# Kernel optimization log

Measured on AMD Instinct MI355X. Metric: run time of the kernel, lower is better.

Reference implementation:

```python
import jax, jax.numpy as jnp
import numpy as np

EMBED = 64
HEADS = 8
HEAD_DIM = EMBED // HEADS
B, N, T = 8, 128, 64


def setup_inputs() -> dict:
    key = jax.random.key(0)
    ks = jax.random.split(key, 8)
    shp = (B, N, T, EMBED)
    values = jax.random.normal(ks[0], shp, dtype=jnp.float32)
    keys = jax.random.normal(ks[1], shp, dtype=jnp.float32)
    query = jax.random.normal(ks[2], shp, dtype=jnp.float32)
    s = 1.0 / np.sqrt(HEAD_DIM)
    Wv = jax.random.normal(ks[3], (HEAD_DIM, HEAD_DIM), dtype=jnp.float32) * s
    Wk = jax.random.normal(ks[4], (HEAD_DIM, HEAD_DIM), dtype=jnp.float32) * s
    Wq = jax.random.normal(ks[5], (HEAD_DIM, HEAD_DIM), dtype=jnp.float32) * s
    so = 1.0 / np.sqrt(EMBED)
    Wo = jax.random.normal(ks[6], (EMBED, EMBED), dtype=jnp.float32) * so
    bo = jax.random.normal(ks[7], (EMBED,), dtype=jnp.float32) * 0.01
    return {"values": values, "keys": keys, "query": query,
            "Wv": Wv, "Wk": Wk, "Wq": Wq, "Wo": Wo, "bo": bo}


def reference(values, keys, query, Wv, Wk, Wq, Wo, bo):
    b, n, t, c = query.shape
    h, d = HEADS, HEAD_DIM
    # split heads: (B,N,T,H,D)
    v = values.reshape(b, n, t, h, d)
    k = keys.reshape(b, n, t, h, d)
    q = query.reshape(b, n, t, h, d)
    # per-head linear projections (torch Linear: x @ W.T, no bias)
    v = jnp.einsum('bnthd,ed->bnthe', v, Wv)
    k = jnp.einsum('bnthd,ed->bnthe', k, Wk)
    q = jnp.einsum('bnthd,ed->bnthe', q, Wq)
    # attention over spatial axis N, independent per (t, h)
    energy = jnp.einsum('bqthd,bkthd->bqkth', q, k)  # (B,N,N,T,H)
    attn = jax.nn.softmax(energy / jnp.sqrt(jnp.float32(c)), axis=2)
    out = jnp.einsum('bqkth,bkthd->bqthd', attn, v).reshape(b, n, t, h * d)
    # fc_out: x @ Wo.T + bo
    return out @ Wo.T + bo
```

## Files before the change

kernel.cpp:

```cpp
#include <hip/hip_runtime.h>


typedef _Float16 half4 __attribute__((ext_vector_type(4)));
typedef float    f32x4 __attribute__((ext_vector_type(4)));

#define MFMA16(a,b,c) __builtin_amdgcn_mfma_f32_16x16x16f16((a),(b),(c),0,0,0)

__device__ __forceinline__ unsigned short f2h(float f){
    union { _Float16 h; unsigned short u; } c; c.h = (_Float16)f; return c.u;
}

#define ZS 0
#define KB 8
#define QB 8200
#define VB 16392
#define CB 24584
#define WB 33288
#define LDS_TOTAL 37640

__global__ __launch_bounds__(512, 4)
void sattn_kernel(const float* __restrict__ V,
                  const float* __restrict__ K,
                  const float* __restrict__ Q,
                  const float* __restrict__ Wv,
                  const float* __restrict__ Wk,
                  const float* __restrict__ Wq,
                  const float* __restrict__ Wo,
                  const float* __restrict__ bo,
                  float* __restrict__ Out)
{
    __shared__ __align__(16) unsigned short smem[LDS_TOTAL];

    const int tid  = threadIdx.x;
    const int bid  = blockIdx.x;
    const int b    = bid >> 6;
    const int t    = bid & 63;
    const long base = (long)b * 524288 + t * 64;
    const float SC = 0.18033688011112043f;

    if (tid < 4) *(unsigned int*)(smem + tid*2) = 0u;

    {
        int o = tid >> 3, c8 = tid & 7;
        const float* ws = Wo + o*64 + c8*8;
        float4 a = *(const float4*)ws;
        float4 d = *(const float4*)(ws + 4);
        half4 h0; h0.x=(_Float16)a.x; h0.y=(_Float16)a.y; h0.z=(_Float16)a.z; h0.w=(_Float16)a.w;
        half4 h1; h1.x=(_Float16)d.x; h1.y=(_Float16)d.y; h1.z=(_Float16)d.z; h1.w=(_Float16)d.w;
        *(half4*)(smem + WB + o*68 + c8*8)     = h0;
        *(half4*)(smem + WB + o*68 + c8*8 + 4) = h1;
    }

    for (int i = 0; i < 2; ++i){
        int id = i*512 + tid;
        int cn = id >> 3, ch = id & 7;
        const float* pk = K + base + cn*4096 + ch*8;
        const float* pv = V + base + cn*4096 + ch*8;
        const float* pq = Q + base + cn*4096 + ch*8;
        float4 ka = *(const float4*)pk, kb = *(const float4*)(pk+4);
        float4 va = *(const float4*)pv, vb = *(const float4*)(pv+4);
        float4 qa = *(const float4*)pq, qb = *(const float4*)(pq+4);
        float ok[8], ov[8], oq[8];
        #pragma unroll
        for (int e = 0; e < 8; ++e){
            float4 wk0 = *(const float4*)(Wk + e*8), wk1 = *(const float4*)(Wk + e*8 + 4);
            float4 wv0 = *(const float4*)(Wv + e*8), wv1 = *(const float4*)(Wv + e*8 + 4);
            float4 wq0 = *(const float4*)(Wq + e*8), wq1 = *(const float4*)(Wq + e*8 + 4);
            ok[e] = ka.x*wk0.x + ka.y*wk0.y + ka.z*wk0.z + ka.w*wk0.w
                  + kb.x*wk1.x + kb.y*wk1.y + kb.z*wk1.z + kb.w*wk1.w;
            ov[e] = va.x*wv0.x + va.y*wv0.y + va.z*wv0.z + va.w*wv0.w
                  + vb.x*wv1.x + vb.y*wv1.y + vb.z*wv1.z + vb.w*wv1.w;
            oq[e] = (qa.x*wq0.x + qa.y*wq0.y + qa.z*wq0.z + qa.w*wq0.w
                  +  qb.x*wq1.x + qb.y*wq1.y + qb.z*wq1.z + qb.w*wq1.w) * SC;
        }
        half4 k0; k0.x=(_Float16)ok[0]; k0.y=(_Float16)ok[1]; k0.z=(_Float16)ok[2]; k0.w=(_Float16)ok[3];
        half4 k1; k1.x=(_Float16)ok[4]; k1.y=(_Float16)ok[5]; k1.z=(_Float16)ok[6]; k1.w=(_Float16)ok[7];
        half4 q0; q0.x=(_Float16)oq[0]; q0.y=(_Float16)oq[1]; q0.z=(_Float16)oq[2]; q0.w=(_Float16)oq[3];
        half4 q1; q1.x=(_Float16)oq[4]; q1.y=(_Float16)oq[5]; q1.z=(_Float16)oq[6]; q1.w=(_Float16)oq[7];
        *(half4*)(smem + KB + ch*1024 + cn*8)     = k0;
        *(half4*)(smem + KB + ch*1024 + cn*8 + 4) = k1;
        *(half4*)(smem + QB + ch*1024 + cn*8)     = q0;
        *(half4*)(smem + QB + ch*1024 + cn*8 + 4) = q1;
        #pragma unroll
        for (int e = 0; e < 8; ++e)
            smem[VB + ch*1024 + e*128 + cn] = f2h(ov[e]);
    }

    __syncthreads();

    const int h    = tid >> 6;
    const int q16  = tid & 15;
    const int quad = (tid & 63) >> 4;
    const f32x4 zz = {0.f, 0.f, 0.f, 0.f};

    half4 kf[8];
    #pragma unroll
    for (int mt = 0; mt < 8; ++mt){
        int a = KB + h*1024 + (mt*16 + q16)*8 + quad*4;
        if (quad >= 2) a = ZS;
        kf[mt] = *(const half4*)(smem + a);
    }
    half4 vf[8];
    #pragma unroll
    for (int s = 0; s < 8; ++s){
        int a = VB + h*1024 + q16*128 + s*16 + quad*4;
        if (q16 >= 8) a = ZS;
        vf[s] = *(const half4*)(smem + a);
    }

    #pragma unroll 1
    for (int qs = 0; qs < 8; ++qs){
        int qa = QB + h*1024 + (qs*16 + q16)*8 + quad*4;
        if (quad >= 2) qa = ZS;
        half4 qf = *(const half4*)(smem + qa);

        f32x4 acc[8];
        #pragma unroll
        for (int mt = 0; mt < 8; ++mt)
            acc[mt] = MFMA16(kf[mt], qf, zz);

        float s = 0.f;
        #pragma unroll
        for (int mt = 0; mt < 8; ++mt){
            #pragma unroll
            for (int r = 0; r < 4; ++r){
                float p = __builtin_amdgcn_exp2f(acc[mt][r]);
                acc[mt][r] = p;
                s += p;
            }
        }
        s += __shfl_xor(s, 16, 64);
        s += __shfl_xor(s, 32, 64);
        float inv = 1.0f / s;

        half4 pf[8];
        #pragma unroll
        for (int mt = 0; mt < 8; ++mt){
            pf[mt].x = (_Float16)(acc[mt][0]*inv);
            pf[mt].y = (_Float16)(acc[mt][1]*inv);
            pf[mt].z = (_Float16)(acc[mt][2]*inv);
            pf[mt].w = (_Float16)(acc[mt][3]*inv);
        }

        f32x4 o = zz;
        #pragma unroll
        for (int s8 = 0; s8 < 8; ++s8)
            o = MFMA16(pf[s8], vf[s8], o);

        if (q16 < 8){
            #pragma unroll
            for (int r = 0; r < 4; ++r){
                int row = qs*16 + quad*4 + r;
                smem[CB + row*68 + h*8 + q16] = f2h(o[r]);
            }
        }
    }

    __syncthreads();

    const int w = h;
    half4 af[4];
    #pragma unroll
    for (int ks = 0; ks < 4; ++ks)
        af[ks] = *(const half4*)(smem + CB + (w*16 + q16)*68 + ks*16 + quad*4);

    #pragma unroll
    for (int nt = 0; nt < 4; ++nt){
        f32x4 a = zz;
        #pragma unroll
        for (int ks = 0; ks < 4; ++ks){
            half4 bf = *(const half4*)(smem + WB + (nt*16 + q16)*68 + ks*16 + quad*4);
            a = MFMA16(af[ks], bf, a);
        }
        float bb = bo[nt*16 + q16];
        #pragma unroll
        for (int r = 0; r < 4; ++r){
            int row = w*16 + quad*4 + r;
            Out[base + (long)row*4096 + nt*16 + q16] = a[r] + bb;
        }
    }
}

extern "C" void kernel_launch(void* const* d_in, const int* in_sizes, int n_in,
                              void* d_out, int out_size, void* d_ws, size_t ws_size,
                              hipStream_t stream)
{
    const float* V  = (const float*)d_in[0];
    const float* K  = (const float*)d_in[1];
    const float* Q  = (const float*)d_in[2];
    const float* Wv = (const float*)d_in[3];
    const float* Wk = (const float*)d_in[4];
    const float* Wq = (const float*)d_in[5];
    const float* Wo = (const float*)d_in[6];
    const float* bo = (const float*)d_in[7];

    sattn_kernel<<<dim3(512), dim3(512), 0, stream>>>(
        V, K, Q, Wv, Wk, Wq, Wo, bo, (float*)d_out);
}
```

Baseline: 114.8 us.

## Defer softmax normalization past PV MFMA, batch global loads, pack fp16 conversions

```diff
diff --git a/kernel.cpp b/kernel.cpp
--- a/kernel.cpp
+++ b/kernel.cpp
@@ -2,12 +2,18 @@
 
 
 typedef _Float16 half4 __attribute__((ext_vector_type(4)));
+typedef __fp16   fp16x2 __attribute__((ext_vector_type(2)));
 typedef float    f32x4 __attribute__((ext_vector_type(4)));
 
 #define MFMA16(a,b,c) __builtin_amdgcn_mfma_f32_16x16x16f16((a),(b),(c),0,0,0)
 
 __device__ __forceinline__ unsigned short f2h(float f){
     union { _Float16 h; unsigned short u; } c; c.h = (_Float16)f; return c.u;
+}
+__device__ __forceinline__ unsigned int pk2(float a, float b){
+    union { fp16x2 h; unsigned int u; } c;
+    c.h = __builtin_amdgcn_cvt_pkrtz(a, b);
+    return c.u;
 }
 
 #define ZS 0
@@ -15,8 +21,8 @@
 #define QB 8200
 #define VB 16392
 #define CB 24584
-#define WB 33288
-#define LDS_TOTAL 37640
+#define WB 33800
+#define LDS_TOTAL 38408
 
 __global__ __launch_bounds__(512, 4)
 void sattn_kernel(const float* __restrict__ V,
@@ -45,45 +51,52 @@
         const float* ws = Wo + o*64 + c8*8;
         float4 a = *(const float4*)ws;
         float4 d = *(const float4*)(ws + 4);
-        half4 h0; h0.x=(_Float16)a.x; h0.y=(_Float16)a.y; h0.z=(_Float16)a.z; h0.w=(_Float16)a.w;
-        half4 h1; h1.x=(_Float16)d.x; h1.y=(_Float16)d.y; h1.z=(_Float16)d.z; h1.w=(_Float16)d.w;
-        *(half4*)(smem + WB + o*68 + c8*8)     = h0;
-        *(half4*)(smem + WB + o*68 + c8*8 + 4) = h1;
-    }
-
-    for (int i = 0; i < 2; ++i){
-        int id = i*512 + tid;
-        int cn = id >> 3, ch = id & 7;
-        const float* pk = K + base + cn*4096 + ch*8;
-        const float* pv = V + base + cn*4096 + ch*8;
-        const float* pq = Q + base + cn*4096 + ch*8;
-        float4 ka = *(const float4*)pk, kb = *(const float4*)(pk+4);
-        float4 va = *(const float4*)pv, vb = *(const float4*)(pv+4);
-        float4 qa = *(const float4*)pq, qb = *(const float4*)(pq+4);
-        float ok[8], ov[8], oq[8];
-        #pragma unroll
-        for (int e = 0; e < 8; ++e){
-            float4 wk0 = *(const float4*)(Wk + e*8), wk1 = *(const float4*)(Wk + e*8 + 4);
-            float4 wv0 = *(const float4*)(Wv + e*8), wv1 = *(const float4*)(Wv + e*8 + 4);
-            float4 wq0 = *(const float4*)(Wq + e*8), wq1 = *(const float4*)(Wq + e*8 + 4);
-            ok[e] = ka.x*wk0.x + ka.y*wk0.y + ka.z*wk0.z + ka.w*wk0.w
-                  + kb.x*wk1.x + kb.y*wk1.y + kb.z*wk1.z + kb.w*wk1.w;
-            ov[e] = va.x*wv0.x + va.y*wv0.y + va.z*wv0.z + va.w*wv0.w
-                  + vb.x*wv1.x + vb.y*wv1.y + vb.z*wv1.z + vb.w*wv1.w;
-            oq[e] = (qa.x*wq0.x + qa.y*wq0.y + qa.z*wq0.z + qa.w*wq0.w
-                  +  qb.x*wq1.x + qb.y*wq1.y + qb.z*wq1.z + qb.w*wq1.w) * SC;
-        }
-        half4 k0; k0.x=(_Float16)ok[0]; k0.y=(_Float16)ok[1]; k0.z=(_Float16)ok[2]; k0.w=(_Float16)ok[3];
-        half4 k1; k1.x=(_Float16)ok[4]; k1.y=(_Float16)ok[5]; k1.z=(_Float16)ok[6]; k1.w=(_Float16)ok[7];
-        half4 q0; q0.x=(_Float16)oq[0]; q0.y=(_Float16)oq[1]; q0.z=(_Float16)oq[2]; q0.w=(_Float16)oq[3];
-        half4 q1; q1.x=(_Float16)oq[4]; q1.y=(_Float16)oq[5]; q1.z=(_Float16)oq[6]; q1.w=(_Float16)oq[7];
-        *(half4*)(smem + KB + ch*1024 + cn*8)     = k0;
-        *(half4*)(smem + KB + ch*1024 + cn*8 + 4) = k1;
-        *(half4*)(smem + QB + ch*1024 + cn*8)     = q0;
-        *(half4*)(smem + QB + ch*1024 + cn*8 + 4) = q1;
-        #pragma unroll
-        for (int e = 0; e < 8; ++e)
-            smem[VB + ch*1024 + e*128 + cn] = f2h(ov[e]);
+        *(uint4*)(smem + WB + o*72 + c8*8) =
+            make_uint4(pk2(a.x,a.y), pk2(a.z,a.w), pk2(d.x,d.y), pk2(d.z,d.w));
+    }
+
+    {
+        float4 L[12];
+        int cn_[2], ch_[2];
+        #pragma unroll
+        for (int i = 0; i < 2; ++i){
+            int id = i*512 + tid;
+            int cn = id >> 3, ch = id & 7;
+            cn_[i] = cn; ch_[i] = ch;
+            const float* pk = K + base + cn*4096 + ch*8;
+            const float* pv = V + base + cn*4096 + ch*8;
+            const float* pq = Q + base + cn*4096 + ch*8;
+            L[i*6+0] = *(const float4*)pk;  L[i*6+1] = *(const float4*)(pk+4);
+            L[i*6+2] = *(const float4*)pv;  L[i*6+3] = *(const float4*)(pv+4);
+            L[i*6+4] = *(const float4*)pq;  L[i*6+5] = *(const float4*)(pq+4);
+        }
+        #pragma unroll
+        for (int i = 0; i < 2; ++i){
+            int cn = cn_[i], ch = ch_[i];
+            float4 ka = L[i*6+0], kb = L[i*6+1];
+            float4 va = L[i*6+2], vb = L[i*6+3];
+            float4 qa = L[i*6+4], qb = L[i*6+5];
+            float ok[8], ov[8], oq[8];
+            #pragma unroll
+            for (int e = 0; e < 8; ++e){
+                float4 wk0 = *(const float4*)(Wk + e*8), wk1 = *(const float4*)(Wk + e*8 + 4);
+                float4 wv0 = *(const float4*)(Wv + e*8), wv1 = *(const float4*)(Wv + e*8 + 4);
+                float4 wq0 = *(const float4*)(Wq + e*8), wq1 = *(const float4*)(Wq + e*8 + 4);
+                ok[e] = ka.x*wk0.x + ka.y*wk0.y + ka.z*wk0.z + ka.w*wk0.w
+                      + kb.x*wk1.x + kb.y*wk1.y + kb.z*wk1.z + kb.w*wk1.w;
+                ov[e] = va.x*wv0.x + va.y*wv0.y + va.z*wv0.z + va.w*wv0.w
+                      + vb.x*wv1.x + vb.y*wv1.y + vb.z*wv1.z + vb.w*wv1.w;
+                oq[e] = (qa.x*wq0.x + qa.y*wq0.y + qa.z*wq0.z + qa.w*wq0.w
+                      +  qb.x*wq1.x + qb.y*wq1.y + qb.z*wq1.z + qb.w*wq1.w) * SC;
+            }
+            *(uint4*)(smem + KB + ch*1024 + cn*8) =
+                make_uint4(pk2(ok[0],ok[1]), pk2(ok[2],ok[3]), pk2(ok[4],ok[5]), pk2(ok[6],ok[7]));
+            *(uint4*)(smem + QB + ch*1024 + cn*8) =
+                make_uint4(pk2(oq[0],oq[1]), pk2(oq[2],oq[3]), pk2(oq[4],oq[5]), pk2(oq[6],oq[7]));
+            #pragma unroll
+            for (int e = 0; e < 8; ++e)
+                smem[VB + ch*1024 + e*128 + cn] = f2h(ov[e]);
+        }
     }
 
     __syncthreads();
@@ -107,51 +120,56 @@
         if (q16 >= 8) a = ZS;
         vf[s] = *(const half4*)(smem + a);
     }
+    half4 qf[8];
+    #pragma unroll
+    for (int qs = 0; qs < 8; ++qs){
+        int a = QB + h*1024 + (qs*16 + q16)*8 + quad*4;
+        if (quad >= 2) a = ZS;
+        qf[qs] = *(const half4*)(smem + a);
+    }
 
     #pragma unroll 1
     for (int qs = 0; qs < 8; ++qs){
-        int qa = QB + h*1024 + (qs*16 + q16)*8 + quad*4;
-        if (quad >= 2) qa = ZS;
-        half4 qf = *(const half4*)(smem + qa);
-
         f32x4 acc[8];
         #pragma unroll
         for (int mt = 0; mt < 8; ++mt)
-            acc[mt] = MFMA16(kf[mt], qf, zz);
+            acc[mt] = MFMA16(kf[mt], qf[qs], zz);
 
         float s = 0.f;
         #pragma unroll
         for (int mt = 0; mt < 8; ++mt){
             #pragma unroll
             for (int r = 0; r < 4; ++r){
-                float p = __builtin_amdgcn_exp2f(acc[mt][r]);
+                float p = __builtin_amdgcn_exp2f(fminf(acc[mt][r], 14.f));
                 acc[mt][r] = p;
                 s += p;
             }
         }
+
+        union { uint2 u; half4 hp; } pf[8];
+        #pragma unroll
+        for (int mt = 0; mt < 8; ++mt)
+            pf[mt].u = make_uint2(pk2(acc[mt][0], acc[mt][1]),
+                                  pk2(acc[mt][2], acc[mt][3]));
+
         s += __shfl_xor(s, 16, 64);
         s += __shfl_xor(s, 32, 64);
         float inv = 1.0f / s;
-
-        half4 pf[8];
-        #pragma unroll
-        for (int mt = 0; mt < 8; ++mt){
-            pf[mt].x = (_Float16)(acc[mt][0]*inv);
-            pf[mt].y = (_Float16)(acc[mt][1]*inv);
-            pf[mt].z = (_Float16)(acc[mt][2]*inv);
-            pf[mt].w = (_Float16)(acc[mt][3]*inv);
-        }
+        float invr[4];
+        #pragma unroll
+        for (int r = 0; r < 4; ++r)
+            invr[r] = __shfl(inv, quad*4 + r, 64);
 
         f32x4 o = zz;
         #pragma unroll
         for (int s8 = 0; s8 < 8; ++s8)
-            o = MFMA16(pf[s8], vf[s8], o);
+            o = MFMA16(pf[s8].hp, vf[s8], o);
 
         if (q16 < 8){
             #pragma unroll
             for (int r = 0; r < 4; ++r){
                 int row = qs*16 + quad*4 + r;
-                smem[CB + row*68 + h*8 + q16] = f2h(o[r]);
+                smem[CB + row*72 + h*8 + q16] = f2h(o[r] * invr[r]);
             }
         }
     }
@@ -162,14 +180,14 @@
     half4 af[4];
     #pragma unroll
     for (int ks = 0; ks < 4; ++ks)
-        af[ks] = *(const half4*)(smem + CB + (w*16 + q16)*68 + ks*16 + quad*4);
+        af[ks] = *(const half4*)(smem + CB + (w*16 + q16)*72 + ks*16 + quad*4);
 
     #pragma unroll
     for (int nt = 0; nt < 4; ++nt){
         f32x4 a = zz;
         #pragma unroll
         for (int ks = 0; ks < 4; ++ks){
-            half4 bf = *(const half4*)(smem + WB + (nt*16 + q16)*68 + ks*16 + quad*4);
+            half4 bf = *(const half4*)(smem + WB + (nt*16 + q16)*72 + ks*16 + quad*4);
             a = MFMA16(af[ks], bf, a);
         }
         float bb = bo[nt*16 + q16];
```

Result: slower. 129.3 us (+12.6%).
